# Kernel optimization log

Hardware: AMD Instinct MI355X
Metric: run time of the kernel (lower is better)

## Reference

```python
import jax, jax.numpy as jnp
import numpy as np

N, E, H = 50000, 800000, 128
EPS = 1e-7      # GENConv message epsilon
BN_EPS = 1e-5
LN_EPS = 1e-5

def setup_inputs() -> dict:
    key = jax.random.key(0)
    ks = jax.random.split(key, 12)
    return dict(
        h=jax.random.normal(ks[0], (N, H), jnp.float32),
        edge_index=jax.random.randint(ks[1], (2, E), 0, N, dtype=jnp.int32),
        edge_attr=jax.random.normal(ks[2], (E, H), jnp.float32),
        bn_weight=1.0 + 0.1 * jax.random.normal(ks[3], (H,), jnp.float32),
        bn_bias=0.1 * jax.random.normal(ks[4], (H,), jnp.float32),
        bn_mean=0.1 * jax.random.normal(ks[5], (H,), jnp.float32),
        bn_var=jax.random.uniform(ks[6], (H,), jnp.float32, 0.5, 1.5),
        t=jnp.array(1.0, jnp.float32),  # learnable softmax temperature
        W1=jax.random.normal(ks[7], (H, 2 * H), jnp.float32) / np.float32(np.sqrt(H)),
        b1=jnp.zeros((2 * H,), jnp.float32),
        ln_weight=jnp.ones((2 * H,), jnp.float32),
        ln_bias=jnp.zeros((2 * H,), jnp.float32),
        W2=jax.random.normal(ks[8], (2 * H, H), jnp.float32) / np.float32(np.sqrt(2 * H)),
        b2=jnp.zeros((H,), jnp.float32),
    )

def reference(h, edge_index, edge_attr, bn_weight, bn_bias, bn_mean, bn_var,
              t, W1, b1, ln_weight, ln_bias, W2, b2):
    x = h
    # DeepGCNLayer 'res+' pre-block: BatchNorm (eval, running stats) -> ReLU
    hn = (x - bn_mean) * jax.lax.rsqrt(bn_var + BN_EPS) * bn_weight + bn_bias
    hn = jax.nn.relu(hn)

    src, dst = edge_index[0], edge_index[1]
    # GENConv message: relu(x_j + edge_attr) + eps  -> [E, H]
    msg = jax.nn.relu(hn[src] + edge_attr) + EPS

    # softmax aggregation per destination node (per feature channel)
    logits = msg * t
    seg_max = jax.ops.segment_max(jax.lax.stop_gradient(logits), dst, num_segments=N)
    seg_max = jnp.where(jnp.isfinite(seg_max), seg_max, 0.0)
    ex = jnp.exp(logits - seg_max[dst])
    denom = jax.ops.segment_sum(ex, dst, num_segments=N)
    alpha = ex / (denom[dst] + 1e-16)
    agg = jax.ops.segment_sum(msg * alpha, dst, num_segments=N)  # [N, H]

    # GENConv: out = mlp(aggr + x_r)
    out = agg + hn
    y = out @ W1 + b1                               # [N, 2H]
    mu = y.mean(-1, keepdims=True)
    var = ((y - mu) ** 2).mean(-1, keepdims=True)
    y = (y - mu) * jax.lax.rsqrt(var + LN_EPS) * ln_weight + ln_bias
    y = jax.nn.relu(y)
    y = y @ W2 + b2                                 # [N, H]

    # res+ residual
    return x + y
```

## Files before the change

### kernel.cpp

```cpp
#include <hip/hip_runtime.h>

#define NN 50000
#define HH 128
#define EE 800000

__global__ __launch_bounds__(256) void init_kernel(
    const float* __restrict__ h,
    const float* __restrict__ bnw,
    const float* __restrict__ bnb,
    const float* __restrict__ bnm,
    const float* __restrict__ bnv,
    float* __restrict__ hn,
    int*   __restrict__ deg)
{
    int i4 = blockIdx.x * 256 + threadIdx.x;
    int c4 = i4 & 31;
    const float4 wv = ((const float4*)bnw)[c4];
    const float4 bv = ((const float4*)bnb)[c4];
    const float4 mv = ((const float4*)bnm)[c4];
    const float4 vv = ((const float4*)bnv)[c4];
    const float4 xv = ((const float4*)h)[i4];
    float4 r;
    r.x = fmaxf((xv.x - mv.x) * rsqrtf(vv.x + 1e-5f) * wv.x + bv.x, 0.f);
    r.y = fmaxf((xv.y - mv.y) * rsqrtf(vv.y + 1e-5f) * wv.y + bv.y, 0.f);
    r.z = fmaxf((xv.z - mv.z) * rsqrtf(vv.z + 1e-5f) * wv.z + bv.z, 0.f);
    r.w = fmaxf((xv.w - mv.w) * rsqrtf(vv.w + 1e-5f) * wv.w + bv.w, 0.f);
    ((float4*)hn)[i4] = r;
    if (i4 < NN) deg[i4] = 0;
}

__global__ __launch_bounds__(256) void hist_kernel(
    const int* __restrict__ ei, int* __restrict__ deg)
{
    int e = blockIdx.x * 256 + threadIdx.x;
    atomicAdd(&deg[ei[EE + e]], 1);
}

__global__ __launch_bounds__(1024) void scan_kernel(
    const int* __restrict__ deg, int* __restrict__ rowptr)
{
    __shared__ int part[1024];
    const int t = threadIdx.x;
    const int CH = 49;
    int lo = t * CH, hi = min(lo + CH, NN);
    int s = 0;
    for (int i = lo; i < hi; ++i) s += deg[i];
    part[t] = s;
    __syncthreads();
    for (int off = 1; off < 1024; off <<= 1) {
        int v = (t >= off) ? part[t - off] : 0;
        __syncthreads();
        part[t] += v;
        __syncthreads();
    }
    int run = part[t] - s;
    for (int i = lo; i < hi; ++i) { rowptr[i] = run; run += deg[i]; }
}

__global__ __launch_bounds__(256) void scatter_kernel(
    const int* __restrict__ ei, int* __restrict__ rowptr,
    int2* __restrict__ pair)
{
    int e = blockIdx.x * 256 + threadIdx.x;
    int src = ei[e];
    int dst = ei[EE + e];
    int pos = atomicAdd(&rowptr[dst], 1);
    pair[pos] = make_int2(e, src);
}

__global__ __launch_bounds__(256) void gather_kernel(
    const float* __restrict__ hn,
    const float* __restrict__ ea,
    const int*   __restrict__ rowptr,
    const int*   __restrict__ deg,
    const int2*  __restrict__ pair,
    const float* __restrict__ tptr,
    float* __restrict__ aggskip)
{
    const int wave = threadIdx.x >> 6;
    const int lane = threadIdx.x & 63;
    const int n = blockIdx.x * 4 + wave;
    const int end   = rowptr[n];
    const int d     = deg[n];
    const int start = end - d;
    const float t = tptr[0];
    const int c = lane * 2;

    float d0 = 0.f, d1 = 0.f, n0 = 0.f, n1 = 0.f;

    int2 pr_next;
    if (start < end) pr_next = pair[start];
    for (int i = start; i < end; ++i) {
        int2 pr = pr_next;
        if (i + 1 < end) pr_next = pair[i + 1];
        const float2 a  = *(const float2*)(ea + (size_t)pr.x * HH + c);
        const float2 hv = *(const float2*)(hn + (size_t)pr.y * HH + c);
        float m0 = fmaxf(hv.x + a.x, 0.f) + 1e-7f;
        float m1 = fmaxf(hv.y + a.y, 0.f) + 1e-7f;
        float e0 = __expf(m0 * t);
        float e1 = __expf(m1 * t);
        d0 += e0; d1 += e1;
        n0 += m0 * e0; n1 += m1 * e1;
    }

    size_t g = (size_t)n * HH + c;
    const float2 hown = *(const float2*)(hn + g);
    float2 r;
    r.x = n0 / (d0 + 1e-16f) + hown.x;
    r.y = n1 / (d1 + 1e-16f) + hown.y;
    *(float2*)(aggskip + g) = r;
}

#define SY 272
__global__ __launch_bounds__(256) void mlp_kernel(
    const float* __restrict__ h,
    const float* __restrict__ aggskip,
    const float* __restrict__ W1,
    const float* __restrict__ b1,
    const float* __restrict__ lnw,
    const float* __restrict__ lnb,
    const float* __restrict__ W2,
    const float* __restrict__ b2,
    float* __restrict__ out)
{
    __shared__ float s_out[16][128];
    __shared__ float s_y[16 * SY];
    __shared__ float s_mu[16], s_rs[16];

    const int tid = threadIdx.x;
    const int nb  = blockIdx.x * 16;

    #pragma unroll
    for (int p = 0; p < 8; ++p) {
        int idx = tid + p * 256;
        int n = idx >> 7, k = idx & 127;
        s_out[n][k] = aggskip[(size_t)(nb + n) * HH + k];
    }
    __syncthreads();

    {
        float bj = b1[tid];
        float acc[16];
        #pragma unroll
        for (int n = 0; n < 16; ++n) acc[n] = bj;
        for (int k = 0; k < 128; ++k) {
            float wv = W1[k * 256 + tid];
            #pragma unroll
            for (int n = 0; n < 16; ++n) acc[n] += s_out[n][k] * wv;
        }
        #pragma unroll
        for (int n = 0; n < 16; ++n) s_y[n * SY + tid] = acc[n];
    }
    __syncthreads();

    {
        int grp = tid >> 4, l16 = tid & 15;
        float s = 0.f, sq = 0.f;
        for (int j = l16; j < 256; j += 16) {
            float v = s_y[grp * SY + j];
            s += v; sq += v * v;
        }
        #pragma unroll
        for (int off = 8; off > 0; off >>= 1) {
            s  += __shfl_down(s,  off, 16);
            sq += __shfl_down(sq, off, 16);
        }
        if (l16 == 0) {
            float mu  = s * (1.f / 256.f);
            float var = sq * (1.f / 256.f) - mu * mu;
            s_mu[grp] = mu;
            s_rs[grp] = rsqrtf(var + 1e-5f);
        }
    }
    __syncthreads();

    {
        float lw = lnw[tid], lb = lnb[tid];
        #pragma unroll
        for (int n = 0; n < 16; ++n) {
            float v = (s_y[n * SY + tid] - s_mu[n]) * s_rs[n] * lw + lb;
            s_y[n * SY + tid] = fmaxf(v, 0.f);
        }
    }
    __syncthreads();

    {
        int j  = tid & 127;
        int n0 = (tid >> 7) * 8;
        float b2j = b2[j];
        float acc2[8];
        #pragma unroll
        for (int m = 0; m < 8; ++m) acc2[m] = b2j;
        for (int k = 0; k < 256; ++k) {
            float wv = W2[k * 128 + j];
            #pragma unroll
            for (int m = 0; m < 8; ++m) acc2[m] += s_y[(n0 + m) * SY + k] * wv;
        }
        #pragma unroll
        for (int m = 0; m < 8; ++m) {
            size_t g = (size_t)(nb + n0 + m) * HH + j;
            out[g] = h[g] + acc2[m];
        }
    }
}

extern "C" void kernel_launch(void* const* d_in, const int* in_sizes, int n_in,
                              void* d_out, int out_size, void* d_ws, size_t ws_size,
                              hipStream_t stream)
{
    const float* h   = (const float*)d_in[0];
    const int*   ei  = (const int*)d_in[1];
    const float* ea  = (const float*)d_in[2];
    const float* bnw = (const float*)d_in[3];
    const float* bnb = (const float*)d_in[4];
    const float* bnm = (const float*)d_in[5];
    const float* bnv = (const float*)d_in[6];
    const float* t   = (const float*)d_in[7];
    const float* W1  = (const float*)d_in[8];
    const float* b1  = (const float*)d_in[9];
    const float* lnw = (const float*)d_in[10];
    const float* lnb = (const float*)d_in[11];
    const float* W2  = (const float*)d_in[12];
    const float* b2  = (const float*)d_in[13];
    float* out = (float*)d_out;

    const size_t NH = (size_t)NN * HH;
    char* base = (char*)d_ws;
    float* hn     = (float*)base;
    int*   deg    = (int*)(base + NH * sizeof(float));
    int*   rowptr = (int*)(base + NH * sizeof(float) + 200000);
    int2*  pair   = (int2*)(base + NH * sizeof(float) + 400000);
    float* aggskip = out;

    init_kernel<<<(int)(NH / 1024), 256, 0, stream>>>(h, bnw, bnb, bnm, bnv, hn, deg);
    hist_kernel<<<EE / 256, 256, 0, stream>>>(ei, deg);
    scan_kernel<<<1, 1024, 0, stream>>>(deg, rowptr);
    scatter_kernel<<<EE / 256, 256, 0, stream>>>(ei, rowptr, pair);
    gather_kernel<<<NN / 4, 256, 0, stream>>>(hn, ea, rowptr, deg, pair, t, aggskip);
    mlp_kernel<<<NN / 16, 256, 0, stream>>>(h, aggskip, W1, b1, lnw, lnb, W2, b2, out);
}
```

Measured before the change: 928.1 us.

## Use bf16 MFMA for MLP, split edges across half-waves, shuffle-based scan

Rewrites the node MLP to run both matmuls on bf16 MFMA instructions, with a new kernel that pre-transposes and converts W1/W2 to bf16 and uses XOR-swizzled LDS tiles. The layer-norm statistics now come from cross-lane shuffles instead of a shared-memory pass. The gather kernel has each half-wave process alternate edges with float4 loads and combines the halves at the end. The scan uses wave shuffles instead of a 1024-wide LDS Hillis-Steele loop. Rounding activations and weights to bf16 lowers matmul precision.

```diff
diff --git a/kernel.cpp b/kernel.cpp
--- a/kernel.cpp
+++ b/kernel.cpp
@@ -3,6 +3,15 @@
 #define NN 50000
 #define HH 128
 #define EE 800000
+
+typedef __attribute__((ext_vector_type(8))) short bf16x8;
+typedef __attribute__((ext_vector_type(4))) float f32x4;
+
+__device__ __forceinline__ short f2b(float f) {
+    unsigned u = __float_as_uint(f);
+    unsigned r = (u + 0x7fffu + ((u >> 16) & 1u)) >> 16;
+    return (short)r;
+}
 
 __global__ __launch_bounds__(256) void init_kernel(
     const float* __restrict__ h,
@@ -29,6 +38,21 @@
     if (i4 < NN) deg[i4] = 0;
 }
 
+__global__ __launch_bounds__(256) void convert_kernel(
+    const float* __restrict__ W1, const float* __restrict__ W2,
+    short* __restrict__ W1T, short* __restrict__ W2T)
+{
+    int id = blockIdx.x * 256 + threadIdx.x;
+    if (id < 32768) {
+        int c = id >> 7, k = id & 127;
+        W1T[id] = f2b(W1[k * 256 + c]);
+    } else {
+        int j = id - 32768;
+        int c = j >> 8, k = j & 255;
+        W2T[j] = f2b(W2[k * 128 + c]);
+    }
+}
+
 __global__ __launch_bounds__(256) void hist_kernel(
     const int* __restrict__ ei, int* __restrict__ deg)
 {
@@ -39,21 +63,33 @@
 __global__ __launch_bounds__(1024) void scan_kernel(
     const int* __restrict__ deg, int* __restrict__ rowptr)
 {
-    __shared__ int part[1024];
+    __shared__ int wsum[16];
     const int t = threadIdx.x;
+    const int lane = t & 63, wid = t >> 6;
     const int CH = 49;
     int lo = t * CH, hi = min(lo + CH, NN);
     int s = 0;
     for (int i = lo; i < hi; ++i) s += deg[i];
-    part[t] = s;
-    __syncthreads();
-    for (int off = 1; off < 1024; off <<= 1) {
-        int v = (t >= off) ? part[t - off] : 0;
-        __syncthreads();
-        part[t] += v;
-        __syncthreads();
-    }
-    int run = part[t] - s;
+    int val = s;
+    #pragma unroll
+    for (int off = 1; off < 64; off <<= 1) {
+        int u = __shfl_up(val, off, 64);
+        if (lane >= off) val += u;
+    }
+    if (lane == 63) wsum[wid] = val;
+    __syncthreads();
+    if (t < 16) {
+        int v = wsum[t];
+        #pragma unroll
+        for (int off = 1; off < 16; off <<= 1) {
+            int u = __shfl_up(v, off, 16);
+            if ((t & 15) >= off) v += u;
+        }
+        wsum[t] = v;
+    }
+    __syncthreads();
+    int base = (wid > 0 ? wsum[wid - 1] : 0) + (val - s);
+    int run = base;
     for (int i = lo; i < hi; ++i) { rowptr[i] = run; run += deg[i]; }
 }
 
@@ -81,125 +117,179 @@
     const int lane = threadIdx.x & 63;
     const int n = blockIdx.x * 4 + wave;
     const int end   = rowptr[n];
-    const int d     = deg[n];
-    const int start = end - d;
+    const int start = end - deg[n];
     const float t = tptr[0];
-    const int c = lane * 2;
-
-    float d0 = 0.f, d1 = 0.f, n0 = 0.f, n1 = 0.f;
-
+    const int c = (lane & 31) * 4;
+    const int epar = lane >> 5;
+
+    float4 dn = make_float4(0.f, 0.f, 0.f, 0.f);
+    float4 nm = make_float4(0.f, 0.f, 0.f, 0.f);
+
+    int i = start + epar;
     int2 pr_next;
-    if (start < end) pr_next = pair[start];
-    for (int i = start; i < end; ++i) {
+    if (i < end) pr_next = pair[i];
+    for (; i < end; i += 2) {
         int2 pr = pr_next;
-        if (i + 1 < end) pr_next = pair[i + 1];
-        const float2 a  = *(const float2*)(ea + (size_t)pr.x * HH + c);
-        const float2 hv = *(const float2*)(hn + (size_t)pr.y * HH + c);
+        if (i + 2 < end) pr_next = pair[i + 2];
+        const float4 a  = *(const float4*)(ea + (size_t)pr.x * HH + c);
+        const float4 hv = *(const float4*)(hn + (size_t)pr.y * HH + c);
         float m0 = fmaxf(hv.x + a.x, 0.f) + 1e-7f;
         float m1 = fmaxf(hv.y + a.y, 0.f) + 1e-7f;
+        float m2 = fmaxf(hv.z + a.z, 0.f) + 1e-7f;
+        float m3 = fmaxf(hv.w + a.w, 0.f) + 1e-7f;
         float e0 = __expf(m0 * t);
         float e1 = __expf(m1 * t);
-        d0 += e0; d1 += e1;
-        n0 += m0 * e0; n1 += m1 * e1;
-    }
-
-    size_t g = (size_t)n * HH + c;
-    const float2 hown = *(const float2*)(hn + g);
-    float2 r;
-    r.x = n0 / (d0 + 1e-16f) + hown.x;
-    r.y = n1 / (d1 + 1e-16f) + hown.y;
-    *(float2*)(aggskip + g) = r;
-}
-
-#define SY 272
+        float e2 = __expf(m2 * t);
+        float e3 = __expf(m3 * t);
+        dn.x += e0; dn.y += e1; dn.z += e2; dn.w += e3;
+        nm.x += m0 * e0; nm.y += m1 * e1; nm.z += m2 * e2; nm.w += m3 * e3;
+    }
+    dn.x += __shfl_xor(dn.x, 32); dn.y += __shfl_xor(dn.y, 32);
+    dn.z += __shfl_xor(dn.z, 32); dn.w += __shfl_xor(dn.w, 32);
+    nm.x += __shfl_xor(nm.x, 32); nm.y += __shfl_xor(nm.y, 32);
+    nm.z += __shfl_xor(nm.z, 32); nm.w += __shfl_xor(nm.w, 32);
+
+    if (lane < 32) {
+        size_t g = (size_t)n * HH + c;
+        const float4 hown = *(const float4*)(hn + g);
+        float4 r;
+        r.x = nm.x / (dn.x + 1e-16f) + hown.x;
+        r.y = nm.y / (dn.y + 1e-16f) + hown.y;
+        r.z = nm.z / (dn.z + 1e-16f) + hown.z;
+        r.w = nm.w / (dn.w + 1e-16f) + hown.w;
+        *(float4*)(aggskip + g) = r;
+    }
+}
+
 __global__ __launch_bounds__(256) void mlp_kernel(
     const float* __restrict__ h,
     const float* __restrict__ aggskip,
-    const float* __restrict__ W1,
+    const short* __restrict__ W1T,
     const float* __restrict__ b1,
     const float* __restrict__ lnw,
     const float* __restrict__ lnb,
-    const float* __restrict__ W2,
+    const short* __restrict__ W2T,
     const float* __restrict__ b2,
     float* __restrict__ out)
 {
-    __shared__ float s_out[16][128];
-    __shared__ float s_y[16 * SY];
+    __shared__ __align__(16) short As[16 * 128];
+    __shared__ __align__(16) short Yb[16 * 256];
+    __shared__ float pS[4][16], pQ[4][16];
     __shared__ float s_mu[16], s_rs[16];
 
     const int tid = threadIdx.x;
+    const int w   = tid >> 6;
+    const int l   = tid & 63;
+    const int l15 = l & 15;
+    const int lg  = l >> 4;
     const int nb  = blockIdx.x * 16;
 
-    #pragma unroll
-    for (int p = 0; p < 8; ++p) {
-        int idx = tid + p * 256;
-        int n = idx >> 7, k = idx & 127;
-        s_out[n][k] = aggskip[(size_t)(nb + n) * HH + k];
-    }
-    __syncthreads();
-
     {
-        float bj = b1[tid];
-        float acc[16];
-        #pragma unroll
-        for (int n = 0; n < 16; ++n) acc[n] = bj;
-        for (int k = 0; k < 128; ++k) {
-            float wv = W1[k * 256 + tid];
-            #pragma unroll
-            for (int n = 0; n < 16; ++n) acc[n] += s_out[n][k] * wv;
-        }
-        #pragma unroll
-        for (int n = 0; n < 16; ++n) s_y[n * SY + tid] = acc[n];
-    }
-    __syncthreads();
-
-    {
-        int grp = tid >> 4, l16 = tid & 15;
-        float s = 0.f, sq = 0.f;
-        for (int j = l16; j < 256; j += 16) {
-            float v = s_y[grp * SY + j];
-            s += v; sq += v * v;
-        }
-        #pragma unroll
-        for (int off = 8; off > 0; off >>= 1) {
-            s  += __shfl_down(s,  off, 16);
-            sq += __shfl_down(sq, off, 16);
-        }
-        if (l16 == 0) {
-            float mu  = s * (1.f / 256.f);
-            float var = sq * (1.f / 256.f) - mu * mu;
-            s_mu[grp] = mu;
-            s_rs[grp] = rsqrtf(var + 1e-5f);
-        }
-    }
-    __syncthreads();
-
-    {
-        float lw = lnw[tid], lb = lnb[tid];
-        #pragma unroll
-        for (int n = 0; n < 16; ++n) {
-            float v = (s_y[n * SY + tid] - s_mu[n]) * s_rs[n] * lw + lb;
-            s_y[n * SY + tid] = fmaxf(v, 0.f);
-        }
-    }
-    __syncthreads();
-
-    {
-        int j  = tid & 127;
-        int n0 = (tid >> 7) * 8;
-        float b2j = b2[j];
-        float acc2[8];
-        #pragma unroll
-        for (int m = 0; m < 8; ++m) acc2[m] = b2j;
-        for (int k = 0; k < 256; ++k) {
-            float wv = W2[k * 128 + j];
-            #pragma unroll
-            for (int m = 0; m < 8; ++m) acc2[m] += s_y[(n0 + m) * SY + k] * wv;
-        }
-        #pragma unroll
-        for (int m = 0; m < 8; ++m) {
-            size_t g = (size_t)(nb + n0 + m) * HH + j;
-            out[g] = h[g] + acc2[m];
+        int row  = tid >> 4;
+        int colb = (tid & 15) * 8;
+        const float4* src = (const float4*)(aggskip + (size_t)(nb + row) * HH + colb);
+        float4 v0 = src[0], v1 = src[1];
+        bf16x8 pk;
+        pk[0] = f2b(v0.x); pk[1] = f2b(v0.y); pk[2] = f2b(v0.z); pk[3] = f2b(v0.w);
+        pk[4] = f2b(v1.x); pk[5] = f2b(v1.y); pk[6] = f2b(v1.z); pk[7] = f2b(v1.w);
+        int sb = (row * 256 + colb * 2) ^ ((row & 7) << 4);
+        *(bf16x8*)((char*)As + sb) = pk;
+    }
+    __syncthreads();
+
+    bf16x8 af[4];
+    #pragma unroll
+    for (int ks = 0; ks < 4; ++ks) {
+        int off = (lg * 16 + ks * 64) ^ ((l15 & 7) << 4);
+        af[ks] = *(bf16x8*)((char*)As + l15 * 256 + off);
+    }
+    f32x4 acc[4];
+    #pragma unroll
+    for (int nt = 0; nt < 4; ++nt) {
+        int col = w * 64 + nt * 16 + l15;
+        const short* bp = W1T + col * 128 + lg * 8;
+        f32x4 a = {0.f, 0.f, 0.f, 0.f};
+        #pragma unroll
+        for (int ks = 0; ks < 4; ++ks) {
+            bf16x8 bfr = *(const bf16x8*)(bp + ks * 32);
+            a = __builtin_amdgcn_mfma_f32_16x16x32_bf16(af[ks], bfr, a, 0, 0, 0);
+        }
+        acc[nt] = a;
+    }
+
+    float b1c[4];
+    #pragma unroll
+    for (int nt = 0; nt < 4; ++nt) b1c[nt] = b1[w * 64 + nt * 16 + l15];
+    #pragma unroll
+    for (int i = 0; i < 4; ++i) {
+        float s = 0.f, q = 0.f;
+        #pragma unroll
+        for (int nt = 0; nt < 4; ++nt) {
+            float v = acc[nt][i] + b1c[nt];
+            acc[nt][i] = v;
+            s += v; q += v * v;
+        }
+        s += __shfl_xor(s, 1); q += __shfl_xor(q, 1);
+        s += __shfl_xor(s, 2); q += __shfl_xor(q, 2);
+        s += __shfl_xor(s, 4); q += __shfl_xor(q, 4);
+        s += __shfl_xor(s, 8); q += __shfl_xor(q, 8);
+        if (l15 == 0) { pS[w][lg * 4 + i] = s; pQ[w][lg * 4 + i] = q; }
+    }
+    __syncthreads();
+    if (tid < 16) {
+        float S = pS[0][tid] + pS[1][tid] + pS[2][tid] + pS[3][tid];
+        float Q = pQ[0][tid] + pQ[1][tid] + pQ[2][tid] + pQ[3][tid];
+        float mu  = S * (1.f / 256.f);
+        float var = Q * (1.f / 256.f) - mu * mu;
+        s_mu[tid] = mu;
+        s_rs[tid] = rsqrtf(var + 1e-5f);
+    }
+    __syncthreads();
+
+    #pragma unroll
+    for (int nt = 0; nt < 4; ++nt) {
+        int col = w * 64 + nt * 16 + l15;
+        float lw = lnw[col], lb = lnb[col];
+        #pragma unroll
+        for (int i = 0; i < 4; ++i) {
+            int r = lg * 4 + i;
+            float v = (acc[nt][i] - s_mu[r]) * s_rs[r] * lw + lb;
+            v = fmaxf(v, 0.f);
+            int sb = (r * 512 + col * 2) ^ ((r & 7) << 4);
+            *(short*)((char*)Yb + sb) = f2b(v);
+        }
+    }
+    __syncthreads();
+
+    bf16x8 a2[8];
+    #pragma unroll
+    for (int ks = 0; ks < 8; ++ks) {
+        int off = (lg * 16 + ks * 64) ^ ((l15 & 7) << 4);
+        a2[ks] = *(bf16x8*)((char*)Yb + l15 * 512 + off);
+    }
+    f32x4 acc2[2];
+    #pragma unroll
+    for (int nt = 0; nt < 2; ++nt) {
+        int col = w * 32 + nt * 16 + l15;
+        const short* bp = W2T + col * 256 + lg * 8;
+        f32x4 a = {0.f, 0.f, 0.f, 0.f};
+        #pragma unroll
+        for (int ks = 0; ks < 8; ++ks) {
+            bf16x8 bfr = *(const bf16x8*)(bp + ks * 32);
+            a = __builtin_amdgcn_mfma_f32_16x16x32_bf16(a2[ks], bfr, a, 0, 0, 0);
+        }
+        acc2[nt] = a;
+    }
+
+    #pragma unroll
+    for (int nt = 0; nt < 2; ++nt) {
+        int col = w * 32 + nt * 16 + l15;
+        float bb = b2[col];
+        #pragma unroll
+        for (int i = 0; i < 4; ++i) {
+            int r = lg * 4 + i;
+            size_t g = (size_t)(nb + r) * HH + col;
+            out[g] = h[g] + acc2[nt][i] + bb;
         }
     }
 }
@@ -227,15 +317,18 @@
     const size_t NH = (size_t)NN * HH;
     char* base = (char*)d_ws;
     float* hn     = (float*)base;
-    int*   deg    = (int*)(base + NH * sizeof(float));
-    int*   rowptr = (int*)(base + NH * sizeof(float) + 200000);
-    int2*  pair   = (int2*)(base + NH * sizeof(float) + 400000);
+    int*   deg    = (int*)(base + NH * 4);
+    int*   rowptr = (int*)(base + NH * 4 + 200000);
+    int2*  pair   = (int2*)(base + NH * 4 + 400000);
+    short* W1T = (short*)(base + NH * 4 + 400000 + (size_t)EE * 8);
+    short* W2T = W1T + 32768;
     float* aggskip = out;
 
     init_kernel<<<(int)(NH / 1024), 256, 0, stream>>>(h, bnw, bnb, bnm, bnv, hn, deg);
+    convert_kernel<<<256, 256, 0, stream>>>(W1, W2, W1T, W2T);
     hist_kernel<<<EE / 256, 256, 0, stream>>>(ei, deg);
     scan_kernel<<<1, 1024, 0, stream>>>(deg, rowptr);
     scatter_kernel<<<EE / 256, 256, 0, stream>>>(ei, rowptr, pair);
     gather_kernel<<<NN / 4, 256, 0, stream>>>(hn, ea, rowptr, deg, pair, t, aggskip);
-    mlp_kernel<<<NN / 16, 256, 0, stream>>>(h, aggskip, W1, b1, lnw, lnb, W2, b2, out);
-}
+    mlp_kernel<<<NN / 16, 256, 0, stream>>>(h, aggskip, W1T, b1, lnw, lnb, W2T, b2, out);
+}
```

Result: faster. 813.1 us (-12.4%).
